# Kernel optimization log

Hardware: AMD Instinct MI355X
Metric: run time of the kernel (lower is better)

## Reference

```python
import jax, jax.numpy as jnp
from jax import lax
import numpy as np

FEAT_STRIDE = 16
RATIOS = np.array([0.5, 1.0, 2.0])
SCALES = np.array([8.0, 16.0, 32.0])
PRE_NMS = 6000
POST_NMS = 300
NMS_THRESH = 0.7
MIN_SIZE = 16.0
A = 9  # num anchors per location


def _whctrs(a):
    w = a[2] - a[0] + 1.0
    h = a[3] - a[1] + 1.0
    return w, h, a[0] + 0.5 * (w - 1.0), a[1] + 0.5 * (h - 1.0)


def _mkanchors(ws, hs, cx, cy):
    return np.stack([cx - 0.5 * (ws - 1.0), cy - 0.5 * (hs - 1.0),
                     cx + 0.5 * (ws - 1.0), cy + 0.5 * (hs - 1.0)], axis=1)


def generate_anchors(base_size=16):
    base = np.array([1.0, 1.0, base_size, base_size]) - 1.0
    w, h, cx, cy = _whctrs(base)
    size = w * h
    ws = np.round(np.sqrt(size / RATIOS))
    hs = np.round(ws * RATIOS)
    ratio_anchors = _mkanchors(ws, hs, cx, cy)
    out = []
    for ra in ratio_anchors:
        w, h, cx, cy = _whctrs(ra)
        out.append(_mkanchors(w * SCALES, h * SCALES, cx, cy))
    return np.concatenate(out, axis=0).astype(np.float32)  # [9,4]


def setup_inputs() -> dict:
    key = jax.random.key(0)
    k1, k2 = jax.random.split(key)
    scores = jax.random.normal(k1, (1, 2 * A, 50, 80), dtype=jnp.float32)
    bbox_deltas = jax.random.normal(k2, (1, 4 * A, 50, 80), dtype=jnp.float32) * 0.5
    im_info = jnp.array([[800.0, 1280.0, 1.5]], dtype=jnp.float32)  # (h, w, scale)
    return {"scores": scores, "bbox_deltas": bbox_deltas, "im_info": im_info}


def reference(scores, bbox_deltas, im_info):
    base_anchors = jnp.asarray(generate_anchors())  # [A,4]
    H, W = scores.shape[-2], scores.shape[-1]

    # fg scores, flattened in (h, w, a) order to match anchor ordering
    sc = scores[:, A:, :, :].transpose(0, 2, 3, 1).reshape(-1)  # [K*A]

    # anchors for every feature-map location
    sx = (jnp.arange(W) * FEAT_STRIDE).astype(jnp.float32)
    sy = (jnp.arange(H) * FEAT_STRIDE).astype(jnp.float32)
    gy, gx = jnp.meshgrid(sy, sx, indexing="ij")
    shifts = jnp.stack([gx, gy, gx, gy], axis=-1).reshape(-1, 1, 4)  # [K,1,4]
    anchors = (base_anchors[None, :, :] + shifts).reshape(-1, 4)    # [K*A,4]

    # decode deltas (dw/dh clamped to [-10,10])
    d = bbox_deltas.transpose(0, 2, 3, 1).reshape(-1, 4)
    d = jnp.concatenate([d[:, :2], jnp.clip(d[:, 2:], -10.0, 10.0)], axis=1)
    aw = anchors[:, 2] - anchors[:, 0] + 1.0
    ah = anchors[:, 3] - anchors[:, 1] + 1.0
    acx = anchors[:, 0] + 0.5 * aw
    acy = anchors[:, 1] + 0.5 * ah
    pcx = d[:, 0] * aw + acx
    pcy = d[:, 1] * ah + acy
    pw = jnp.exp(d[:, 2]) * aw
    ph = jnp.exp(d[:, 3]) * ah
    boxes = jnp.stack([pcx - 0.5 * pw, pcy - 0.5 * ph,
                       pcx + 0.5 * pw, pcy + 0.5 * ph], axis=1)

    # clip to image
    im_h, im_w, im_s = im_info[0, 0], im_info[0, 1], im_info[0, 2]
    boxes = jnp.stack([
        jnp.clip(boxes[:, 0], 0.0, im_w - 1.0),
        jnp.clip(boxes[:, 1], 0.0, im_h - 1.0),
        jnp.clip(boxes[:, 2], 0.0, im_w - 1.0),
        jnp.clip(boxes[:, 3], 0.0, im_h - 1.0),
    ], axis=1)

    # min-size filter (masking instead of compaction, for static shapes)
    ws = boxes[:, 2] - boxes[:, 0] + 1.0
    hs = boxes[:, 3] - boxes[:, 1] + 1.0
    min_sz = MIN_SIZE * im_s
    valid = (ws >= min_sz) & (hs >= min_sz)
    sc = jnp.where(valid, sc, -jnp.inf)

    # pre-NMS top-k by score
    top_sc, top_idx = lax.top_k(sc, PRE_NMS)
    props = boxes[top_idx]  # [P,4], sorted by descending score
    alive0 = jnp.isfinite(top_sc)

    # pairwise IoU (the +1 pixel convention matching the rest of the pipeline)
    x1, y1, x2, y2 = props[:, 0], props[:, 1], props[:, 2], props[:, 3]
    areas = (x2 - x1 + 1.0) * (y2 - y1 + 1.0)
    iw = jnp.clip(jnp.minimum(x2[:, None], x2[None, :]) - jnp.maximum(x1[:, None], x1[None, :]) + 1.0, 0.0)
    ih = jnp.clip(jnp.minimum(y2[:, None], y2[None, :]) - jnp.maximum(y1[:, None], y1[None, :]) + 1.0, 0.0)
    inter = iw * ih
    iou = inter / (areas[:, None] + areas[None, :] - inter)  # [P,P] ~144MB

    idx = jnp.arange(PRE_NMS)

    def body(i, keep):
        sup = keep[i] & (iou[i] > NMS_THRESH) & (idx > i)
        return keep & ~sup

    keep = lax.fori_loop(0, PRE_NMS, body, alive0)

    # gather first POST_NMS kept proposals into fixed-size output [POST_NMS,5]
    rank = jnp.cumsum(keep) - 1
    dest = jnp.where(keep & (rank < POST_NMS), rank, POST_NMS)
    out = jnp.zeros((POST_NMS + 1, 5), dtype=scores.dtype)
    out = out.at[dest, 1:].set(props)
    return out[:POST_NMS]
```

## Files before the change

### kernel.cpp

```cpp
#include <hip/hip_runtime.h>
#include <stdint.h>

#define A_NUM 9
#define H_FM 50
#define W_FM 80
#define N_ANCH (A_NUM * H_FM * W_FM)
#define PRE_NMS_N 6000
#define POST_NMS_N 300
#define NMS_TH 0.7f
#define MASK_W 94
#define MASK_STRIDE 96
#define NBIN 4096
#define BIN_CAP 4096
#define NBD 141
#define MASK_TILES (24 * 94)

typedef unsigned long long ull;

__constant__ float c_aw[9] = {184.f,368.f,736.f,128.f,256.f,512.f, 88.f,176.f,352.f};
__constant__ float c_ah[9] = { 96.f,192.f,384.f,128.f,256.f,512.f,176.f,352.f,704.f};

__device__ int    g_hist[NBIN];
__device__ ull    g_dead[MASK_STRIDE];
__device__ ull    g_rowany[MASK_STRIDE];
__device__ float4 g_boxes[N_ANCH];
__device__ float4 g_props[PRE_NMS_N];
__device__ ull    g_mask[(size_t)PRE_NMS_N * MASK_STRIDE];
__device__ ull    g_colsup[MASK_W * 64];

__global__ __launch_bounds__(256) void k_decode(const float* __restrict__ scores,
                                                const float* __restrict__ deltas,
                                                const float* __restrict__ iminfo,
                                                ull* __restrict__ bins) {
    int i = blockIdx.x * 256 + threadIdx.x;
    if (i >= N_ANCH) return;

    int a    = i % A_NUM;
    int cell = i / A_NUM;
    int x    = cell % W_FM;
    int y    = cell / W_FM;
    const int hw = H_FM * W_FM;

    float sc = scores[(A_NUM + a) * hw + cell];

    int dbase = (a * 4) * hw + cell;
    float d0 = deltas[dbase];
    float d1 = deltas[dbase + hw];
    float d2 = deltas[dbase + 2 * hw];
    float d3 = deltas[dbase + 3 * hw];
    d2 = fminf(fmaxf(d2, -10.f), 10.f);
    d3 = fminf(fmaxf(d3, -10.f), 10.f);

    float aw = c_aw[a], ah = c_ah[a];
    float acx = (float)(x * 16 + 8);
    float acy = (float)(y * 16 + 8);

    float pcx = d0 * aw + acx;
    float pcy = d1 * ah + acy;
    float pw  = expf(d2) * aw;
    float ph  = expf(d3) * ah;

    float x1 = pcx - 0.5f * pw;
    float y1 = pcy - 0.5f * ph;
    float x2 = pcx + 0.5f * pw;
    float y2 = pcy + 0.5f * ph;

    float imh = iminfo[0], imw = iminfo[1], ims = iminfo[2];
    x1 = fminf(fmaxf(x1, 0.f), imw - 1.f);
    y1 = fminf(fmaxf(y1, 0.f), imh - 1.f);
    x2 = fminf(fmaxf(x2, 0.f), imw - 1.f);
    y2 = fminf(fmaxf(y2, 0.f), imh - 1.f);

    float wsz = x2 - x1 + 1.f;
    float hsz = y2 - y1 + 1.f;
    float minsz = 16.f * ims;
    bool valid = (wsz >= minsz) && (hsz >= minsz);

    g_boxes[i] = make_float4(x1, y1, x2, y2);

    unsigned int u   = __float_as_uint(sc);
    unsigned int asc = (u & 0x80000000u) ? ~u : (u | 0x80000000u);
    unsigned int dk  = ~asc;
    if (!valid) dk = 0xFF800000u;
    ull key = ((ull)dk << 32) | (unsigned int)i;

    int bin  = (int)(dk >> 20);
    int slot = atomicAdd(&g_hist[bin], 1);
    if (slot < BIN_CAP) bins[(size_t)bin * BIN_CAP + slot] = key;
}

__global__ __launch_bounds__(256) void k_binsort(const ull* __restrict__ bins) {
    __shared__ ull sb[4096];
    __shared__ int red[256];
    int b = blockIdx.x;
    int cntf = g_hist[b];
    if (cntf == 0) return;
    int tid = threadIdx.x;

    int part = 0;
    for (int j = tid; j < b; j += 256) part += g_hist[j];
    red[tid] = part;
    __syncthreads();
    for (int off = 128; off > 0; off >>= 1) {
        if (tid < off) red[tid] += red[tid + off];
        __syncthreads();
    }
    int s0 = red[0];
    if (s0 >= PRE_NMS_N) return;

    int cnt = (cntf < BIN_CAP) ? cntf : BIN_CAP;
    const ull* seg = bins + (size_t)b * BIN_CAP;

    int P = 2; while (P < cnt) P <<= 1;
    for (int i = tid; i < P; i += 256) sb[i] = (i < cnt) ? seg[i] : ~0ULL;
    __syncthreads();
    for (int k2 = 2; k2 <= P; k2 <<= 1) {
        for (int j = k2 >> 1; j >= 1; j >>= 1) {
            for (int p = tid; p < (P >> 1); p += 256) {
                int i  = ((p & ~(j - 1)) << 1) | (p & (j - 1));
                int pr = i | j;
                bool up = ((i & k2) == 0);
                ull a = sb[i], c = sb[pr];
                if ((a > c) == up) { sb[i] = c; sb[pr] = a; }
            }
            __syncthreads();
        }
    }
    for (int i = tid; i < cnt; i += 256) {
        int r = s0 + i;
        if (r < PRE_NMS_N) {
            ull key = sb[i];
            unsigned int dk = (unsigned int)(key >> 32);
            if (dk < 0xFF800000u) {
                g_props[r] = g_boxes[(unsigned int)key];
            } else {
                g_props[r] = make_float4(0.f, 0.f, 0.f, 0.f);
                atomicOr(&g_dead[r >> 6], 1ULL << (r & 63));
            }
        }
    }
}

__global__ __launch_bounds__(256) void k_maskcol() {
    __shared__ float4 sj[256];
    int vb = blockIdx.x;
    int tid = threadIdx.x;

    if (vb < 16) g_hist[vb * 256 + tid] = 0;

    if (vb < MASK_TILES) {
        int bx = vb % 24;
        int by = vb / 24;

        int li = tid & 63;
        int wl = tid >> 6;
        int i  = by * 64 + li;
        int w  = bx * 4 + wl;

        if (bx * 256 + 255 <= by * 64) {
            if (i < PRE_NMS_N && w < MASK_W)
                g_mask[(size_t)i * MASK_STRIDE + w] = 0ULL;
            return;
        }

        int jbase = bx * 256;
        int jj = jbase + tid;
        sj[tid] = (jj < PRE_NMS_N) ? g_props[jj] : make_float4(0.f, 0.f, 0.f, 0.f);
        __syncthreads();

        if (i >= PRE_NMS_N || w >= MASK_W) return;

        float4 bi = g_props[i];
        float ai = (bi.z - bi.x + 1.f) * (bi.w - bi.y + 1.f);
        ull bits = 0;
        int jstart = w * 64;
        int lbase = jstart - jbase;
        int bstart = i + 1 - jstart; if (bstart < 0) bstart = 0;
        int bend = PRE_NMS_N - jstart; if (bend > 64) bend = 64;
        for (int b = bstart; b < bend; ++b) {
            float4 bj = sj[lbase + b];
            float aj = (bj.z - bj.x + 1.f) * (bj.w - bj.y + 1.f);
            float iw = fminf(bi.z, bj.z) - fmaxf(bi.x, bj.x) + 1.f;
            float ih = fminf(bi.w, bj.w) - fmaxf(bi.y, bj.y) + 1.f;
            iw = fmaxf(iw, 0.f);
            ih = fmaxf(ih, 0.f);
            float inter = iw * ih;
            float iou = inter / (ai + aj - inter);
            if (iou > NMS_TH) bits |= (1ULL << b);
        }
        g_mask[(size_t)i * MASK_STRIDE + w] = bits;
        if (bits && w != (i >> 6)) atomicOr(&g_rowany[i >> 6], 1ULL << (i & 63));
    } else {
        int w = vb - MASK_TILES;
        int gj = w * 64 + tid;
        if (tid < 64)
            sj[tid] = (gj < PRE_NMS_N) ? g_props[gj] : make_float4(0.f, 0.f, 0.f, 0.f);
        __syncthreads();
        if (tid < 64) {
            float4 bj = sj[tid];
            float aj = (bj.z - bj.x + 1.f) * (bj.w - bj.y + 1.f);
            ull bits = 0;
            for (int b = 0; b < tid; ++b) {
                float4 bi = sj[b];
                float ai = (bi.z - bi.x + 1.f) * (bi.w - bi.y + 1.f);
                float iw = fminf(bi.z, bj.z) - fmaxf(bi.x, bj.x) + 1.f;
                float ih = fminf(bi.w, bj.w) - fmaxf(bi.y, bj.y) + 1.f;
                iw = fmaxf(iw, 0.f);
                ih = fmaxf(ih, 0.f);
                float inter = iw * ih;
                float iou = inter / (ai + aj - inter);
                if (iou > NMS_TH) bits |= (1ULL << b);
            }
            g_colsup[gj] = bits;
        }
    }
}

#define BATCH 8
__global__ __launch_bounds__(256, 1) void k_scan(float* __restrict__ out) {
    __shared__ ull scol[MASK_W * 64];
    __shared__ ull srow[MASK_W];
    __shared__ int s_kept[POST_NMS_N];
    __shared__ int s_kc;
    int tid = threadIdx.x;

    for (int i = tid; i < MASK_W * 64; i += 256) scol[i] = g_colsup[i];
    for (int i = tid; i < MASK_W; i += 256)      srow[i] = g_rowany[i];
    __syncthreads();

    if (tid < 64) {
        int lane = tid;
        ull rm0 = g_dead[lane];
        ull rm1 = (lane < MASK_W - 64) ? g_dead[64 + lane] : ~0ULL;
        if (lane == 29) rm1 |= 0xFFFF000000000000ULL;
        int kc = 0;

        for (;;) {
            ull avail0 = __ballot(~rm0 != 0ULL);
            ull avail1 = __ballot(~rm1 != 0ULL);
            int w;
            if (avail0)      w = __ffsll(avail0) - 1;
            else if (avail1) w = 63 + __ffsll(avail1);
            else break;

            ull diag = scol[(w << 6) + lane];
            ull raw  = srow[w];
            ull curw = (w < 64) ? __shfl(rm0, w) : __shfl(rm1, w - 64);

            ull U = ~curw;
            ull K = 0;
            while (U) {
                ull UK = U | K;
                bool deadp = (diag & K)  != 0ULL;
                bool freep = (diag & UK) == 0ULL;
                ull nd = __ballot(deadp) & U;
                U &= ~nd;
                ull nk = __ballot(freep) & U;
                U &= ~nk;
                K |= nk;
                if (!nk && !nd) break;
            }

            int cnt  = __popcll(K);
            int take = min(cnt, POST_NMS_N - kc);
            if (K & (1ULL << lane)) {
                int pos = kc + __popcll(K & ((1ULL << lane) - 1ULL));
                if (pos < POST_NMS_N) s_kept[pos] = (w << 6) + lane;
            }
            kc += take;
            if (kc >= POST_NMS_N) break;

            if (w < 64) { if (lane == w)      rm0 = ~0ULL; }
            else        { if (lane == w - 64) rm1 = ~0ULL; }

            ull need = K & raw;
            while (need) {
                int id[BATCH];
                int n = 0;
#pragma unroll
                for (int t2 = 0; t2 < BATCH; ++t2) {
                    id[t2] = 0;
                    if (need) { id[t2] = __ffsll(need) - 1; need &= need - 1; n = t2 + 1; }
                }
                ull v0[BATCH], v1[BATCH];
#pragma unroll
                for (int t2 = 0; t2 < BATCH; ++t2) {
                    const ull* __restrict__ row =
                        g_mask + (size_t)((w << 6) + id[t2]) * MASK_STRIDE;
                    v0[t2] = row[lane];
                    v1[t2] = (lane < MASK_W - 64) ? row[64 + lane] : 0ULL;
                }
                ull a0 = 0, a1 = 0;
#pragma unroll
                for (int t2 = 0; t2 < BATCH; ++t2) {
                    ull m = (t2 < n) ? ~0ULL : 0ULL;
                    a0 |= v0[t2] & m;
                    a1 |= v1[t2] & m;
                }
                rm0 |= a0;
                rm1 |= a1;
            }
        }
        if (lane == 0) s_kc = (kc < POST_NMS_N) ? kc : POST_NMS_N;
    }
    __syncthreads();

    for (int i = tid; i < MASK_STRIDE; i += 256) {
        g_dead[i] = 0ULL;
        g_rowany[i] = 0ULL;
    }

    int kcf = s_kc;
    for (int r = tid; r < POST_NMS_N; r += 256) {
        float4 p = make_float4(0.f, 0.f, 0.f, 0.f);
        if (r < kcf) p = g_props[s_kept[r]];
        out[r * 5 + 0] = 0.f;
        out[r * 5 + 1] = p.x;
        out[r * 5 + 2] = p.y;
        out[r * 5 + 3] = p.z;
        out[r * 5 + 4] = p.w;
    }
}

extern "C" void kernel_launch(void* const* d_in, const int* in_sizes, int n_in,
                              void* d_out, int out_size, void* d_ws, size_t ws_size,
                              hipStream_t stream) {
    const float* scores = (const float*)d_in[0];
    const float* deltas = (const float*)d_in[1];
    const float* iminfo = (const float*)d_in[2];
    float* out = (float*)d_out;
    ull* bins = (ull*)d_ws;

    k_decode<<<NBD, 256, 0, stream>>>(scores, deltas, iminfo, bins);
    k_binsort<<<NBIN, 256, 0, stream>>>(bins);
    k_maskcol<<<MASK_TILES + MASK_W, 256, 0, stream>>>();
    k_scan<<<1, 256, 0, stream>>>(out);
}
```

Before: 118.0 us.

## Coalesce decode loads, add coarse histogram, prefetch diag word, use readlane

The decode kernel now assigns threads in anchor-major order so score and delta reads are contiguous per anchor type. The key still carries the (h,w,a) index, and the box gather maps it back. A 64-bin coarse histogram is added so the prefix sum in binsort reads far fewer entries, at the cost of an extra atomic per anchor. The scan loop prefetches the next diagonal word from shared memory and replaces a 64-bit shuffle with two readlane ops to cut latency on the serial path.

```diff
diff --git a/kernel.cpp b/kernel.cpp
--- a/kernel.cpp
+++ b/kernel.cpp
@@ -4,7 +4,8 @@
 #define A_NUM 9
 #define H_FM 50
 #define W_FM 80
-#define N_ANCH (A_NUM * H_FM * W_FM)
+#define HW (H_FM * W_FM)
+#define N_ANCH (A_NUM * HW)
 #define PRE_NMS_N 6000
 #define POST_NMS_N 300
 #define NMS_TH 0.7f
@@ -21,6 +22,7 @@
 __constant__ float c_ah[9] = { 96.f,192.f,384.f,128.f,256.f,512.f,176.f,352.f,704.f};
 
 __device__ int    g_hist[NBIN];
+__device__ int    g_hist64[64];
 __device__ ull    g_dead[MASK_STRIDE];
 __device__ ull    g_rowany[MASK_STRIDE];
 __device__ float4 g_boxes[N_ANCH];
@@ -32,22 +34,20 @@
                                                 const float* __restrict__ deltas,
                                                 const float* __restrict__ iminfo,
                                                 ull* __restrict__ bins) {
-    int i = blockIdx.x * 256 + threadIdx.x;
-    if (i >= N_ANCH) return;
-
-    int a    = i % A_NUM;
-    int cell = i / A_NUM;
+    int t = blockIdx.x * 256 + threadIdx.x;
+    if (t >= N_ANCH) return;
+    int a    = t / HW;
+    int cell = t - a * HW;
     int x    = cell % W_FM;
     int y    = cell / W_FM;
-    const int hw = H_FM * W_FM;
-
-    float sc = scores[(A_NUM + a) * hw + cell];
-
-    int dbase = (a * 4) * hw + cell;
+
+    float sc = scores[(A_NUM + a) * HW + cell];
+
+    int dbase = (a * 4) * HW + cell;
     float d0 = deltas[dbase];
-    float d1 = deltas[dbase + hw];
-    float d2 = deltas[dbase + 2 * hw];
-    float d3 = deltas[dbase + 3 * hw];
+    float d1 = deltas[dbase + HW];
+    float d2 = deltas[dbase + 2 * HW];
+    float d3 = deltas[dbase + 3 * HW];
     d2 = fminf(fmaxf(d2, -10.f), 10.f);
     d3 = fminf(fmaxf(d3, -10.f), 10.f);
 
@@ -76,16 +76,19 @@
     float minsz = 16.f * ims;
     bool valid = (wsz >= minsz) && (hsz >= minsz);
 
-    g_boxes[i] = make_float4(x1, y1, x2, y2);
+    g_boxes[t] = make_float4(x1, y1, x2, y2);
 
     unsigned int u   = __float_as_uint(sc);
     unsigned int asc = (u & 0x80000000u) ? ~u : (u | 0x80000000u);
     unsigned int dk  = ~asc;
     if (!valid) dk = 0xFF800000u;
-    ull key = ((ull)dk << 32) | (unsigned int)i;
+
+    unsigned int ikey = (unsigned int)(cell * A_NUM + a);
+    ull key = ((ull)dk << 32) | ikey;
 
     int bin  = (int)(dk >> 20);
     int slot = atomicAdd(&g_hist[bin], 1);
+    atomicAdd(&g_hist64[bin >> 6], 1);
     if (slot < BIN_CAP) bins[(size_t)bin * BIN_CAP + slot] = key;
 }
 
@@ -97,8 +100,10 @@
     if (cntf == 0) return;
     int tid = threadIdx.x;
 
+    int cb = b >> 6;
     int part = 0;
-    for (int j = tid; j < b; j += 256) part += g_hist[j];
+    for (int c = tid; c < cb; c += 256) part += g_hist64[c];
+    for (int j = (cb << 6) + tid; j < b; j += 256) part += g_hist[j];
     red[tid] = part;
     __syncthreads();
     for (int off = 128; off > 0; off >>= 1) {
@@ -132,7 +137,9 @@
             ull key = sb[i];
             unsigned int dk = (unsigned int)(key >> 32);
             if (dk < 0xFF800000u) {
-                g_props[r] = g_boxes[(unsigned int)key];
+                unsigned int ik = (unsigned int)key;
+                int tt = (int)(ik % A_NUM) * HW + (int)(ik / A_NUM);
+                g_props[r] = g_boxes[tt];
             } else {
                 g_props[r] = make_float4(0.f, 0.f, 0.f, 0.f);
                 atomicOr(&g_dead[r >> 6], 1ULL << (r & 63));
@@ -147,6 +154,7 @@
     int tid = threadIdx.x;
 
     if (vb < 16) g_hist[vb * 256 + tid] = 0;
+    if (vb == 16 && tid < 64) g_hist64[tid] = 0;
 
     if (vb < MASK_TILES) {
         int bx = vb % 24;
@@ -234,6 +242,8 @@
         ull rm1 = (lane < MASK_W - 64) ? g_dead[64 + lane] : ~0ULL;
         if (lane == 29) rm1 |= 0xFFFF000000000000ULL;
         int kc = 0;
+        int pw = -2;
+        ull dnext = 0;
 
         for (;;) {
             ull avail0 = __ballot(~rm0 != 0ULL);
@@ -243,9 +253,16 @@
             else if (avail1) w = 63 + __ffsll(avail1);
             else break;
 
-            ull diag = scol[(w << 6) + lane];
-            ull raw  = srow[w];
-            ull curw = (w < 64) ? __shfl(rm0, w) : __shfl(rm1, w - 64);
+            ull diag = (w == pw + 1) ? dnext : scol[(w << 6) + lane];
+            if (w + 1 < MASK_W) dnext = scol[((w + 1) << 6) + lane];
+            pw = w;
+
+            ull raw = srow[w];
+            ull rmw = (w < 64) ? rm0 : rm1;
+            int ri  = (w < 64) ? w : w - 64;
+            unsigned clo = __builtin_amdgcn_readlane((unsigned)rmw, ri);
+            unsigned chi = __builtin_amdgcn_readlane((unsigned)(rmw >> 32), ri);
+            ull curw = ((ull)chi << 32) | clo;
 
             ull U = ~curw;
             ull K = 0;
```

Result: slower. 271.7 us (+130.3%).
